# Kernel tuning notes

Measured on AMD Instinct MI355X. Metric: run time of the kernel, lower is better.

## Reference

```python
import jax, jax.numpy as jnp
import numpy as np

B, S, D, H = 2, 2048, 1024, 16
DK = D // H  # 64


def setup_inputs() -> dict:
    key = jax.random.key(0)
    ks = jax.random.split(key, 9)
    query = jax.random.normal(ks[0], (B, S, D), dtype=jnp.float32)
    k_in = jax.random.normal(ks[1], (B, S, D), dtype=jnp.float32)
    v_in = jax.random.normal(ks[2], (B, S, D), dtype=jnp.float32)
    mask = jax.random.randint(ks[3], (B, S, S), 0, 2, dtype=jnp.int32)
    sc = 1.0 / np.sqrt(D)
    Wq = jax.random.normal(ks[4], (H, D, DK), dtype=jnp.float32) * sc  # per-head q proj
    Wk = jax.random.normal(ks[5], (H, D, DK), dtype=jnp.float32) * sc
    Wv = jax.random.normal(ks[6], (H, D, DK), dtype=jnp.float32) * sc
    Wu = jax.random.normal(ks[7], (D, D), dtype=jnp.float32) * sc  # unifyheads weight
    bu = jax.random.normal(ks[8], (D,), dtype=jnp.float32) * 0.01
    return {"query": query, "key": k_in, "value": v_in, "mask": mask,
            "Wq": Wq, "Wk": Wk, "Wv": Wv, "Wu": Wu, "bu": bu}


def reference(query, key, value, mask, Wq, Wk, Wv, Wu, bu):
    scale = DK ** 0.25  # original divides q and k each by d_k^(1/4)
    q = jnp.einsum('bsd,hdk->bhsk', query, Wq) / scale
    k = jnp.einsum('bsd,hdk->bhsk', key, Wk) / scale
    v = jnp.einsum('bsd,hdk->bhsk', value, Wv)
    scores = jnp.einsum('bhsk,bhtk->bhst', q, k)  # [B,H,S,S]
    scores = jnp.where(mask[:, None, :, :] == 0, jnp.float32(-1e9), scores)
    attn = jax.nn.softmax(scores, axis=-1)
    out = jnp.einsum('bhst,bhtk->bhsk', attn, v)
    out = jnp.transpose(out, (0, 2, 1, 3)).reshape(query.shape[0], query.shape[1], D)  # concat heads
    return out @ Wu + bu
```

## Files before the change

kernel.cpp:

```cpp
#include <hip/hip_runtime.h>
#include <hip/hip_bf16.h>


typedef __bf16 bf16_t;
typedef __attribute__((ext_vector_type(4))) __bf16 bf16x4;
typedef __attribute__((ext_vector_type(8))) __bf16 bf16x8;
typedef __attribute__((ext_vector_type(4))) float f32x4;
typedef unsigned int u32;

#define B_ 2
#define S_ 2048
#define D_ 1024
#define H_ 16
#define DK_ 64
#define NX_ (4096 * 1024)

static __device__ __forceinline__ f32x4 mfma16(bf16x8 a, bf16x8 b, f32x4 c) {
  return __builtin_amdgcn_mfma_f32_16x16x32_bf16(a, b, c, 0, 0, 0);
}

static __device__ __forceinline__ void async16(const bf16_t* g, bf16_t* l) {
  __builtin_amdgcn_global_load_lds(
      (const __attribute__((address_space(1))) u32*)g,
      (__attribute__((address_space(3))) u32*)l, 16, 0, 0);
}

__global__ __launch_bounds__(256) void cvt_x(const float* __restrict__ q,
                                             const float* __restrict__ k,
                                             const float* __restrict__ v,
                                             bf16_t* __restrict__ qo,
                                             bf16_t* __restrict__ ko,
                                             bf16_t* __restrict__ vo) {
  const int z = blockIdx.y;
  const float* src = (z == 0) ? q : (z == 1) ? k : v;
  bf16_t* dst = (z == 0) ? qo : (z == 1) ? ko : vo;
  size_t i = ((size_t)blockIdx.x * 256 + threadIdx.x) * 8;
  float4 a = *(const float4*)(src + i);
  float4 b = *(const float4*)(src + i + 4);
  bf16x8 o;
  o[0] = (bf16_t)a.x; o[1] = (bf16_t)a.y; o[2] = (bf16_t)a.z; o[3] = (bf16_t)a.w;
  o[4] = (bf16_t)b.x; o[5] = (bf16_t)b.y; o[6] = (bf16_t)b.z; o[7] = (bf16_t)b.w;
  *(bf16x8*)(dst + i) = o;
}

__global__ __launch_bounds__(256) void wtrans(
    const float* __restrict__ Wq, const float* __restrict__ Wk,
    const float* __restrict__ Wv, const float* __restrict__ Wu,
    bf16_t* __restrict__ Bq, bf16_t* __restrict__ Bk,
    bf16_t* __restrict__ Bv, bf16_t* __restrict__ Bu, float qkscale) {
  __shared__ __align__(16) bf16_t T[64][72];
  const int z = blockIdx.z;
  const float* W = (z == 0) ? Wq : (z == 1) ? Wk : (z == 2) ? Wv : Wu;
  bf16_t* BT = (z == 0) ? Bq : (z == 1) ? Bk : (z == 2) ? Bv : Bu;
  const float scale = (z <= 1) ? qkscale : 1.0f;
  const int d0 = blockIdx.x * 64, nt = blockIdx.y;
  const int tid = threadIdx.x;
  const int r = tid & 63, g = tid >> 6;

  const float* src = (z < 3)
      ? W + ((size_t)nt * D_ + d0 + r) * DK_ + g * 16
      : W + (size_t)(d0 + r) * D_ + nt * 64 + g * 16;
#pragma unroll
  for (int j = 0; j < 4; ++j) {
    float4 w4 = *(const float4*)(src + j * 4);
    T[g * 16 + j * 4 + 0][r] = (bf16_t)(w4.x * scale);
    T[g * 16 + j * 4 + 1][r] = (bf16_t)(w4.y * scale);
    T[g * 16 + j * 4 + 2][r] = (bf16_t)(w4.z * scale);
    T[g * 16 + j * 4 + 3][r] = (bf16_t)(w4.w * scale);
  }
  __syncthreads();
  const int orow = tid >> 3, seg = tid & 7;
#pragma unroll
  for (int p = 0; p < 2; ++p) {
    int rr = p * 32 + orow;
    *(bf16x8*)(BT + (size_t)(nt * 64 + rr) * D_ + d0 + seg * 8) =
        *(const bf16x8*)&T[rr][seg * 8];
  }
}

__global__ __launch_bounds__(256) void vt_build(const bf16_t* __restrict__ V,
                                                bf16_t* __restrict__ Vt) {
  __shared__ __align__(16) bf16_t T[64][72];
  const int r0 = blockIdx.x * 64;
  const int c0 = blockIdx.y * 64;
  const int tid = threadIdx.x;
#pragma unroll
  for (int it = 0; it < 2; ++it) {
    int t = tid + it * 256;
    int rr = t >> 3, cc = (t & 7) * 8;
    *(bf16x8*)&T[rr][cc] = *(const bf16x8*)(V + (size_t)(r0 + rr) * D_ + c0 + cc);
  }
  __syncthreads();
#pragma unroll
  for (int it = 0; it < 2; ++it) {
    int t = tid + it * 256;
    int cr = t >> 3, rc = (t & 7) * 8;
    bf16x8 v;
#pragma unroll
    for (int j = 0; j < 8; ++j) v[j] = T[rc + j][cr];
    *(bf16x8*)(Vt + (size_t)(c0 + cr) * 4096 + r0 + rc) = v;
  }
}

__global__ __launch_bounds__(256) void mask_pack(const int* __restrict__ mask,
                                                 unsigned int* __restrict__ bits) {
  int w = blockIdx.x * 256 + threadIdx.x;
  const int4* p = (const int4*)(mask + (size_t)w * 32);
  unsigned int v = 0;
#pragma unroll
  for (int i = 0; i < 8; ++i) {
    int4 m4 = p[i];
    v |= (m4.x != 0 ? 1u : 0u) << (i * 4 + 0);
    v |= (m4.y != 0 ? 1u : 0u) << (i * 4 + 1);
    v |= (m4.z != 0 ? 1u : 0u) << (i * 4 + 2);
    v |= (m4.w != 0 ? 1u : 0u) << (i * 4 + 3);
  }
  bits[w] = v;
}

__global__ __launch_bounds__(256) void gemm_bt(
    const bf16_t* __restrict__ A0, const bf16_t* __restrict__ A1,
    const bf16_t* __restrict__ A2, const bf16_t* __restrict__ BT0,
    const bf16_t* __restrict__ BT1, const bf16_t* __restrict__ BT2,
    bf16_t* __restrict__ C0, bf16_t* __restrict__ C1, bf16_t* __restrict__ C2) {
  __shared__ __align__(16) bf16_t As[128 * 64];
  __shared__ __align__(16) bf16_t Bs[128 * 64];

  const int z = blockIdx.z;
  const bf16_t* A = (z == 0) ? A0 : (z == 1) ? A1 : A2;
  const bf16_t* BT = (z == 0) ? BT0 : (z == 1) ? BT1 : BT2;
  bf16_t* C = (z == 0) ? C0 : (z == 1) ? C1 : C2;

  const int tid = threadIdx.x;
  const int lane = tid & 63, wave = tid >> 6;
  const int l = lane & 15, quad = lane >> 4;
  const int wm = wave >> 1, wn = wave & 1;
  const int row0 = blockIdx.x * 128, col0 = blockIdx.y * 128;

  const int lr = lane >> 3;
  const int gc8 = (lane & 7) ^ lr;
  const int xl = l & 7;

  f32x4 acc[4][4];
#pragma unroll
  for (int i = 0; i < 4; ++i)
#pragma unroll
    for (int j = 0; j < 4; ++j) acc[i][j] = {0.f, 0.f, 0.f, 0.f};

  for (int k0 = 0; k0 < 1024; k0 += 64) {
    __syncthreads();
#pragma unroll
    for (int c = 0; c < 4; ++c) {
      int r = wave * 32 + c * 8;
      async16(A + (size_t)(row0 + r + lr) * 1024 + k0 + gc8 * 8, As + r * 64);
      async16(BT + (size_t)(col0 + r + lr) * 1024 + k0 + gc8 * 8, Bs + r * 64);
    }
    __syncthreads();

#pragma unroll
    for (int kh = 0; kh < 2; ++kh) {
      bf16x8 af[4], bf[4];
#pragma unroll
      for (int f = 0; f < 4; ++f)
        af[f] = *(const bf16x8*)&As[(wm * 64 + f * 16 + l) * 64 +
                                    (((kh * 4 + quad) ^ xl) * 8)];
#pragma unroll
      for (int f = 0; f < 4; ++f)
        bf[f] = *(const bf16x8*)&Bs[(wn * 64 + f * 16 + l) * 64 +
                                    (((kh * 4 + quad) ^ xl) * 8)];
#pragma unroll
      for (int fm = 0; fm < 4; ++fm)
#pragma unroll
        for (int fn = 0; fn < 4; ++fn)
          acc[fm][fn] = mfma16(af[fm], bf[fn], acc[fm][fn]);
    }
  }

#pragma unroll
  for (int fm = 0; fm < 4; ++fm)
#pragma unroll
    for (int fn = 0; fn < 4; ++fn)
#pragma unroll
      for (int reg = 0; reg < 4; ++reg) {
        int row = row0 + wm * 64 + fm * 16 + quad * 4 + reg;
        int col = col0 + wn * 64 + fn * 16 + l;
        C[(size_t)row * 1024 + col] = (bf16_t)acc[fm][fn][reg];
      }
}

__global__ __launch_bounds__(256) void gemm_bt64(
    const bf16_t* __restrict__ A, const bf16_t* __restrict__ BT,
    float* __restrict__ C, const float* __restrict__ bias) {
  __shared__ __align__(16) bf16_t As[64 * 64];
  __shared__ __align__(16) bf16_t Bs[128 * 64];

  const int tid = threadIdx.x;
  const int lane = tid & 63, wave = tid >> 6;
  const int l = lane & 15, quad = lane >> 4;
  const int row0 = blockIdx.x * 64, col0 = blockIdx.y * 128;

  const int lr = lane >> 3;
  const int gc8 = (lane & 7) ^ lr;
  const int xl = l & 7;

  f32x4 acc[4][2];
#pragma unroll
  for (int i = 0; i < 4; ++i)
#pragma unroll
    for (int j = 0; j < 2; ++j) acc[i][j] = {0.f, 0.f, 0.f, 0.f};

  for (int k0 = 0; k0 < 1024; k0 += 64) {
    __syncthreads();
#pragma unroll
    for (int c = 0; c < 2; ++c) {
      int r = wave * 16 + c * 8;
      async16(A + (size_t)(row0 + r + lr) * 1024 + k0 + gc8 * 8, As + r * 64);
    }
#pragma unroll
    for (int c = 0; c < 4; ++c) {
      int r = wave * 32 + c * 8;
      async16(BT + (size_t)(col0 + r + lr) * 1024 + k0 + gc8 * 8, Bs + r * 64);
    }
    __syncthreads();

#pragma unroll
    for (int kh = 0; kh < 2; ++kh) {
      bf16x8 af[4], bf[2];
#pragma unroll
      for (int f = 0; f < 4; ++f)
        af[f] = *(const bf16x8*)&As[(f * 16 + l) * 64 +
                                    (((kh * 4 + quad) ^ xl) * 8)];
#pragma unroll
      for (int f = 0; f < 2; ++f)
        bf[f] = *(const bf16x8*)&Bs[(wave * 32 + f * 16 + l) * 64 +
                                    (((kh * 4 + quad) ^ xl) * 8)];
#pragma unroll
      for (int fm = 0; fm < 4; ++fm)
#pragma unroll
        for (int fn = 0; fn < 2; ++fn)
          acc[fm][fn] = mfma16(af[fm], bf[fn], acc[fm][fn]);
    }
  }

#pragma unroll
  for (int fm = 0; fm < 4; ++fm)
#pragma unroll
    for (int fn = 0; fn < 2; ++fn)
#pragma unroll
      for (int reg = 0; reg < 4; ++reg) {
        int row = row0 + fm * 16 + quad * 4 + reg;
        int col = col0 + wave * 32 + fn * 16 + l;
        C[(size_t)row * 1024 + col] = acc[fm][fn][reg] + bias[col];
      }
}

__global__ __launch_bounds__(256, 3) void attn_kernel(
    const bf16_t* __restrict__ Qx, const bf16_t* __restrict__ Kx,
    const bf16_t* __restrict__ Vt, const unsigned int* __restrict__ mbits,
    bf16_t* __restrict__ out) {
  __shared__ __align__(16) bf16_t Ks[2][64 * 64];
  __shared__ __align__(16) bf16_t Vts[2][64 * 64];
  __shared__ __align__(16) bf16_t Ps[4][16][72];

  const int tid = threadIdx.x;
  const int lane = tid & 63, wave = tid >> 6;
  const int l = lane & 15, quad = lane >> 4;
  const int qt = blockIdx.x, h = blockIdx.y, b = blockIdx.z;
  const int ch = h * 64;
  const size_t rb = (size_t)b * S_;
  const int q0 = qt * 64 + wave * 16;
  const int quad4 = quad * 4;

  const int lr = lane >> 3;
  const int gc8 = (lane & 7) ^ lr;
  const int xl = l & 7;

  bf16x8 bq[2];
  {
    const bf16_t* qp = Qx + (rb + q0 + l) * D_ + ch;
    bq[0] = *(const bf16x8*)(qp + quad * 8);
    bq[1] = *(const bf16x8*)(qp + 32 + quad * 8);
  }

  bf16x8 ones;
#pragma unroll
  for (int j = 0; j < 8; ++j) ones[j] = (bf16_t)1.0f;

  const f32x4 zero = {0.f, 0.f, 0.f, 0.f};
  f32x4 o[4];
  f32x4 rs = zero;
#pragma unroll
  for (int nt = 0; nt < 4; ++nt) o[nt] = zero;

  const u32* mrow = mbits + (size_t)(b * S_ + q0 + l) * (S_ / 32);

  auto stage = [&](int t0, int buf) {
#pragma unroll
    for (int it = 0; it < 2; ++it) {
      int r0 = it * 32 + wave * 8;
      async16(Kx + (rb + t0 + r0 + lr) * D_ + ch + gc8 * 8,
              &Ks[buf][r0 * 64]);
      async16(Vt + (size_t)(ch + r0 + lr) * 4096 + rb + t0 + gc8 * 8,
              &Vts[buf][r0 * 64]);
    }
  };

  stage(0, 0);
  uint2 mwc = *(const uint2*)&mrow[0];

  int cur = 0;
  for (int t0 = 0; t0 < S_; t0 += 64) {
    __syncthreads();
    const int tn = t0 + 64;
    if (tn < S_) stage(tn, cur ^ 1);
    const int nidx = (tn < S_) ? (tn >> 5) : 0;
    uint2 mwn = *(const uint2*)&mrow[nidx];

    const bf16_t* Kc = Ks[cur];
    const bf16_t* Vc = Vts[cur];

#pragma unroll
    for (int ts = 0; ts < 4; ++ts) {
      int rK = (ts * 16 + l) * 64;
      bf16x8 ak0 = *(const bf16x8*)&Kc[rK + ((quad ^ xl) * 8)];
      bf16x8 ak1 = *(const bf16x8*)&Kc[rK + (((4 + quad) ^ xl) * 8)];
      f32x4 s = mfma16(ak0, bq[0], zero);
      s = mfma16(ak1, bq[1], s);

      u32 mw = (ts < 2) ? mwc.x : mwc.y;
      int base = (ts & 1) * 16 + quad4;
      bf16x4 pv;
#pragma unroll
      for (int reg = 0; reg < 4; ++reg) {
        float e = exp2f(s[reg]);
        int bm = __builtin_amdgcn_sbfe(mw, base + reg, 1);
        float p = __int_as_float(__float_as_int(e) & bm);
        pv[reg] = (bf16_t)p;
      }
      *(bf16x4*)&Ps[wave][l][ts * 16 + quad4] = pv;
    }

    bf16x8 ap0 = *(const bf16x8*)&Ps[wave][l][quad * 8];
    bf16x8 ap1 = *(const bf16x8*)&Ps[wave][l][32 + quad * 8];

    __builtin_amdgcn_s_setprio(1);
    rs = mfma16(ap0, ones, rs);
    rs = mfma16(ap1, ones, rs);
#pragma unroll
    for (int nt = 0; nt < 4; ++nt) {
      int rV = (nt * 16 + l) * 64;
      bf16x8 bv0 = *(const bf16x8*)&Vc[rV + ((quad ^ xl) * 8)];
      bf16x8 bv1 = *(const bf16x8*)&Vc[rV + (((4 + quad) ^ xl) * 8)];
      o[nt] = mfma16(ap0, bv0, o[nt]);
      o[nt] = mfma16(ap1, bv1, o[nt]);
    }
    __builtin_amdgcn_s_setprio(0);

    mwc = mwn;
    cur ^= 1;
  }

#pragma unroll
  for (int reg = 0; reg < 4; ++reg) {
    float inv = (rs[reg] > 0.f) ? (1.f / rs[reg]) : 0.f;
    int srow = q0 + quad4 + reg;
    bf16_t* op = out + (rb + srow) * D_ + ch;
#pragma unroll
    for (int nt = 0; nt < 4; ++nt)
      op[nt * 16 + l] = (bf16_t)(o[nt][reg] * inv);
  }
}

extern "C" void kernel_launch(void* const* d_in, const int* in_sizes, int n_in,
                              void* d_out, int out_size, void* d_ws, size_t ws_size,
                              hipStream_t stream) {
  const float* q_in = (const float*)d_in[0];
  const float* k_in = (const float*)d_in[1];
  const float* v_in = (const float*)d_in[2];
  const int* mask = (const int*)d_in[3];
  const float* Wq = (const float*)d_in[4];
  const float* Wk = (const float*)d_in[5];
  const float* Wv = (const float*)d_in[6];
  const float* Wu = (const float*)d_in[7];
  const float* bu = (const float*)d_in[8];
  float* outp = (float*)d_out;

  bf16_t* qx = (bf16_t*)d_ws;
  bf16_t* kx = qx + NX_;
  bf16_t* vx = kx + NX_;
  bf16_t* qb = vx + NX_;
  bf16_t* kb = qb + NX_;
  bf16_t* vb = kb + NX_;
  bf16_t* BTq = vb + NX_;
  bf16_t* BTk = BTq + D_ * D_;
  bf16_t* BTv = BTk + D_ * D_;
  bf16_t* BTu = BTv + D_ * D_;
  unsigned int* mb = (unsigned int*)(BTu + D_ * D_);
  bf16_t* ab = qx;
  bf16_t* vtb = kx;

  const float qkscale = 0.35355339059327373f * 1.2011224087864498f;

  dim3 blk(256);
  cvt_x<<<dim3(2048, 3), blk, 0, stream>>>(q_in, k_in, v_in, qx, kx, vx);
  wtrans<<<dim3(16, 16, 4), blk, 0, stream>>>(Wq, Wk, Wv, Wu, BTq, BTk, BTv, BTu, qkscale);
  mask_pack<<<dim3(1024), blk, 0, stream>>>(mask, mb);
  gemm_bt<<<dim3(32, 8, 3), blk, 0, stream>>>(qx, kx, vx, BTq, BTk, BTv,
                                              qb, kb, vb);
  vt_build<<<dim3(64, 16), blk, 0, stream>>>(vb, vtb);
  attn_kernel<<<dim3(S_ / 64, H_, B_), dim3(256), 0, stream>>>(qb, kb, vtb, mb, ab);
  gemm_bt64<<<dim3(64, 8), blk, 0, stream>>>(ab, BTu, outp, bu);
}
```

Before: 287.6 us.

## Process 32 query rows per wave in attention and remap blocks across XCDs

Each wave now handles two 16-row query fragments, so every K and V tile loaded into LDS feeds twice as many MFMAs. The grid is halved to 128-row query tiles, and the flat block index is permuted so consecutive blocks of the same head and batch land on the same XCD for L2 reuse. The costs are more registers per wave (launch bounds drop to 2 blocks per SM), a larger P buffer in LDS, and only 512 blocks to spread across the GPU.

After: 273.9 us. 4.8% less time.

```diff
diff --git a/kernel.cpp b/kernel.cpp
--- a/kernel.cpp
+++ b/kernel.cpp
@@ -254,32 +254,39 @@
       }
 }
 
-__global__ __launch_bounds__(256, 3) void attn_kernel(
+__global__ __launch_bounds__(256, 2) void attn_kernel(
     const bf16_t* __restrict__ Qx, const bf16_t* __restrict__ Kx,
     const bf16_t* __restrict__ Vt, const unsigned int* __restrict__ mbits,
     bf16_t* __restrict__ out) {
   __shared__ __align__(16) bf16_t Ks[2][64 * 64];
   __shared__ __align__(16) bf16_t Vts[2][64 * 64];
-  __shared__ __align__(16) bf16_t Ps[4][16][72];
+  __shared__ __align__(16) bf16_t Ps[4][32][72];
 
   const int tid = threadIdx.x;
   const int lane = tid & 63, wave = tid >> 6;
   const int l = lane & 15, quad = lane >> 4;
-  const int qt = blockIdx.x, h = blockIdx.y, b = blockIdx.z;
+
+  const int flat = blockIdx.x + 16 * (blockIdx.y + 16 * blockIdx.z);
+  const int serial = (flat >> 3) + (flat & 7) * 64;
+  const int qt = serial & 15;
+  const int h = (serial >> 4) & 15;
+  const int b = serial >> 8;
+
   const int ch = h * 64;
   const size_t rb = (size_t)b * S_;
-  const int q0 = qt * 64 + wave * 16;
+  const int q0 = qt * 128 + wave * 32;
   const int quad4 = quad * 4;
 
   const int lr = lane >> 3;
   const int gc8 = (lane & 7) ^ lr;
   const int xl = l & 7;
 
-  bf16x8 bq[2];
-  {
-    const bf16_t* qp = Qx + (rb + q0 + l) * D_ + ch;
-    bq[0] = *(const bf16x8*)(qp + quad * 8);
-    bq[1] = *(const bf16x8*)(qp + 32 + quad * 8);
+  bf16x8 bq[2][2];
+#pragma unroll
+  for (int mf = 0; mf < 2; ++mf) {
+    const bf16_t* qp = Qx + (rb + q0 + mf * 16 + l) * D_ + ch;
+    bq[mf][0] = *(const bf16x8*)(qp + quad * 8);
+    bq[mf][1] = *(const bf16x8*)(qp + 32 + quad * 8);
   }
 
   bf16x8 ones;
@@ -287,12 +294,19 @@
   for (int j = 0; j < 8; ++j) ones[j] = (bf16_t)1.0f;
 
   const f32x4 zero = {0.f, 0.f, 0.f, 0.f};
-  f32x4 o[4];
-  f32x4 rs = zero;
-#pragma unroll
-  for (int nt = 0; nt < 4; ++nt) o[nt] = zero;
-
-  const u32* mrow = mbits + (size_t)(b * S_ + q0 + l) * (S_ / 32);
+  f32x4 o[2][4];
+  f32x4 rs[2];
+#pragma unroll
+  for (int mf = 0; mf < 2; ++mf) {
+    rs[mf] = zero;
+#pragma unroll
+    for (int nt = 0; nt < 4; ++nt) o[mf][nt] = zero;
+  }
+
+  const u32* mrow[2];
+#pragma unroll
+  for (int mf = 0; mf < 2; ++mf)
+    mrow[mf] = mbits + (size_t)(b * S_ + q0 + mf * 16 + l) * (S_ / 32);
 
   auto stage = [&](int t0, int buf) {
 #pragma unroll
@@ -306,7 +320,7 @@
   };
 
   stage(0, 0);
-  uint2 mwc = *(const uint2*)&mrow[0];
+  uint2 mwc[2] = {*(const uint2*)&mrow[0][0], *(const uint2*)&mrow[1][0]};
 
   int cur = 0;
   for (int t0 = 0; t0 < S_; t0 += 64) {
@@ -314,7 +328,8 @@
     const int tn = t0 + 64;
     if (tn < S_) stage(tn, cur ^ 1);
     const int nidx = (tn < S_) ? (tn >> 5) : 0;
-    uint2 mwn = *(const uint2*)&mrow[nidx];
+    uint2 mwn0 = *(const uint2*)&mrow[0][nidx];
+    uint2 mwn1 = *(const uint2*)&mrow[1][nidx];
 
     const bf16_t* Kc = Ks[cur];
     const bf16_t* Vc = Vts[cur];
@@ -324,50 +339,66 @@
       int rK = (ts * 16 + l) * 64;
       bf16x8 ak0 = *(const bf16x8*)&Kc[rK + ((quad ^ xl) * 8)];
       bf16x8 ak1 = *(const bf16x8*)&Kc[rK + (((4 + quad) ^ xl) * 8)];
-      f32x4 s = mfma16(ak0, bq[0], zero);
-      s = mfma16(ak1, bq[1], s);
-
-      u32 mw = (ts < 2) ? mwc.x : mwc.y;
       int base = (ts & 1) * 16 + quad4;
-      bf16x4 pv;
-#pragma unroll
-      for (int reg = 0; reg < 4; ++reg) {
-        float e = exp2f(s[reg]);
-        int bm = __builtin_amdgcn_sbfe(mw, base + reg, 1);
-        float p = __int_as_float(__float_as_int(e) & bm);
-        pv[reg] = (bf16_t)p;
+#pragma unroll
+      for (int mf = 0; mf < 2; ++mf) {
+        f32x4 s = mfma16(ak0, bq[mf][0], zero);
+        s = mfma16(ak1, bq[mf][1], s);
+        u32 mw = (ts < 2) ? mwc[mf].x : mwc[mf].y;
+        bf16x4 pv;
+#pragma unroll
+        for (int reg = 0; reg < 4; ++reg) {
+          float e = exp2f(s[reg]);
+          int bm = __builtin_amdgcn_sbfe(mw, base + reg, 1);
+          float p = __int_as_float(__float_as_int(e) & bm);
+          pv[reg] = (bf16_t)p;
+        }
+        *(bf16x4*)&Ps[wave][mf * 16 + l][ts * 16 + quad4] = pv;
       }
-      *(bf16x4*)&Ps[wave][l][ts * 16 + quad4] = pv;
-    }
-
-    bf16x8 ap0 = *(const bf16x8*)&Ps[wave][l][quad * 8];
-    bf16x8 ap1 = *(const bf16x8*)&Ps[wave][l][32 + quad * 8];
+    }
+
+    bf16x8 ap[2][2];
+#pragma unroll
+    for (int mf = 0; mf < 2; ++mf) {
+      ap[mf][0] = *(const bf16x8*)&Ps[wave][mf * 16 + l][quad * 8];
+      ap[mf][1] = *(const bf16x8*)&Ps[wave][mf * 16 + l][32 + quad * 8];
+    }
 
     __builtin_amdgcn_s_setprio(1);
-    rs = mfma16(ap0, ones, rs);
-    rs = mfma16(ap1, ones, rs);
+#pragma unroll
+    for (int mf = 0; mf < 2; ++mf) {
+      rs[mf] = mfma16(ap[mf][0], ones, rs[mf]);
+      rs[mf] = mfma16(ap[mf][1], ones, rs[mf]);
+    }
 #pragma unroll
     for (int nt = 0; nt < 4; ++nt) {
       int rV = (nt * 16 + l) * 64;
       bf16x8 bv0 = *(const bf16x8*)&Vc[rV + ((quad ^ xl) * 8)];
       bf16x8 bv1 = *(const bf16x8*)&Vc[rV + (((4 + quad) ^ xl) * 8)];
-      o[nt] = mfma16(ap0, bv0, o[nt]);
-      o[nt] = mfma16(ap1, bv1, o[nt]);
+#pragma unroll
+      for (int mf = 0; mf < 2; ++mf) {
+        o[mf][nt] = mfma16(ap[mf][0], bv0, o[mf][nt]);
+        o[mf][nt] = mfma16(ap[mf][1], bv1, o[mf][nt]);
+      }
     }
     __builtin_amdgcn_s_setprio(0);
 
-    mwc = mwn;
+    mwc[0] = mwn0;
+    mwc[1] = mwn1;
     cur ^= 1;
   }
 
 #pragma unroll
-  for (int reg = 0; reg < 4; ++reg) {
-    float inv = (rs[reg] > 0.f) ? (1.f / rs[reg]) : 0.f;
-    int srow = q0 + quad4 + reg;
-    bf16_t* op = out + (rb + srow) * D_ + ch;
-#pragma unroll
-    for (int nt = 0; nt < 4; ++nt)
-      op[nt * 16 + l] = (bf16_t)(o[nt][reg] * inv);
+  for (int mf = 0; mf < 2; ++mf) {
+#pragma unroll
+    for (int reg = 0; reg < 4; ++reg) {
+      float inv = (rs[mf][reg] > 0.f) ? (1.f / rs[mf][reg]) : 0.f;
+      int srow = q0 + mf * 16 + quad4 + reg;
+      bf16_t* op = out + (rb + srow) * D_ + ch;
+#pragma unroll
+      for (int nt = 0; nt < 4; ++nt)
+        op[nt * 16 + l] = (bf16_t)(o[mf][nt][reg] * inv);
+    }
   }
 }
 
@@ -408,6 +439,6 @@
   gemm_bt<<<dim3(32, 8, 3), blk, 0, stream>>>(qx, kx, vx, BTq, BTk, BTv,
                                               qb, kb, vb);
   vt_build<<<dim3(64, 16), blk, 0, stream>>>(vb, vtb);
-  attn_kernel<<<dim3(S_ / 64, H_, B_), dim3(256), 0, stream>>>(qb, kb, vtb, mb, ab);
+  attn_kernel<<<dim3(S_ / 128, H_, B_), dim3(256), 0, stream>>>(qb, kb, vtb, mb, ab);
   gemm_bt64<<<dim3(64, 8), blk, 0, stream>>>(ab, BTu, outp, bu);
 }
```
